# Kernel tuning notes

Hardware: AMD Instinct MI355X
Metric: run time of the kernel (lower is better)

Reference implementation:

```python
import jax, jax.numpy as jnp
import numpy as np

B, S, E, H, D = 8, 1024, 1024, 16, 64
LN_EPS = 1e-5


def setup_inputs() -> dict:
    key = jax.random.key(0)
    ks = jax.random.split(key, 8)
    scale = 1.0 / np.sqrt(E)
    return {
        "query": jax.random.normal(ks[0], (B, S, E), jnp.float32),
        "key": jax.random.normal(ks[1], (B, S, E), jnp.float32),
        "value": jax.random.normal(ks[2], (B, S, E), jnp.float32),
        "self_attn_mask": jax.random.randint(ks[3], (B, S, S), 0, 2) == 1,
        "Wq": jax.random.normal(ks[4], (E, H * D), jnp.float32) * scale,
        "Wk": jax.random.normal(ks[5], (E, H * D), jnp.float32) * scale,
        "Wv": jax.random.normal(ks[6], (E, H * D), jnp.float32) * scale,
        "Wo": jax.random.normal(ks[7], (H * D, E), jnp.float32) * scale,
        "ln_gamma": jnp.ones((E,), jnp.float32),
        "ln_beta": jnp.zeros((E,), jnp.float32),
    }


def reference(query, key, value, self_attn_mask, Wq, Wk, Wv, Wo, ln_gamma, ln_beta):
    identity = query
    # project and split heads: [B, S, E] -> [B, H, S, D]
    q = (query @ Wq).reshape(B, S, H, D).transpose(0, 2, 1, 3)
    k = (key @ Wk).reshape(B, S, H, D).transpose(0, 2, 1, 3)
    v = (value @ Wv).reshape(B, S, H, D).transpose(0, 2, 1, 3)
    # scaled dot-product scores in fp32, additive mask fill -1e9
    score = jnp.einsum("bhsd,bhtd->bhst", q, k).astype(jnp.float32) / np.sqrt(D)
    score = jnp.where(self_attn_mask[:, None, :, :], jnp.float32(-1e9), score)
    attn = jax.nn.softmax(score, axis=-1)
    degree = jnp.einsum("bhst,bhtd->bhsd", attn, v)  # [B, H, S, D]
    degree = degree.transpose(0, 2, 1, 3).reshape(B, S, H * D)
    out = degree @ Wo + identity
    # LayerNorm over last dim
    mu = jnp.mean(out, axis=-1, keepdims=True)
    var = jnp.var(out, axis=-1, keepdims=True)
    out = (out - mu) * jax.lax.rsqrt(var + LN_EPS) * ln_gamma + ln_beta
    return out
```

## Files before the change

### kernel.cpp

```cpp
#include <hip/hip_runtime.h>
#include <hip/hip_bf16.h>
#include <cstdint>
#include <cstddef>

typedef __attribute__((ext_vector_type(8))) short bf16x8;
typedef __attribute__((ext_vector_type(8))) unsigned short ushort8;
typedef __attribute__((ext_vector_type(4))) unsigned short ushort4v;
typedef __attribute__((ext_vector_type(4))) float f32x4;

#define B_ 8
#define S_ 1024
#define E_ 1024
#define H_ 16
#define D_ 64
#define NW_ (S_ / 64)

__device__ __forceinline__ unsigned short f2bf(float f) {
    union { float fp; unsigned int u; } v; v.fp = f;
    unsigned int u = v.u;
    return (unsigned short)((u + 0x7fffu + ((u >> 16) & 1u)) >> 16);
}

__device__ __forceinline__ float fexp2(float x) {
    return __builtin_amdgcn_exp2f(x);
}

__device__ __forceinline__ unsigned cvt_pk_bf16(float lo, float hi) {
    unsigned r;
    asm("v_cvt_pk_bf16_f32 %0, %1, %2" : "=v"(r) : "v"(lo), "v"(hi));
    return r;
}

__device__ __forceinline__ void gload16(const void* g, void* l) {
    __builtin_amdgcn_global_load_lds((__attribute__((address_space(1))) void*)g,
                                     (__attribute__((address_space(3))) void*)l,
                                     16, 0, 0);
}

__global__ __launch_bounds__(256) void f32_to_bf16(const float* __restrict__ in,
                                                   unsigned short* __restrict__ out,
                                                   int n8) {
    int i = blockIdx.x * 256 + threadIdx.x;
    const int stride = gridDim.x * 256;
    for (; i < n8; i += stride) {
        float4 f0 = ((const float4*)in)[i * 2];
        float4 f1 = ((const float4*)in)[i * 2 + 1];
        union { unsigned u[4]; ushort8 v; } o;
        o.u[0] = cvt_pk_bf16(f0.x, f0.y);
        o.u[1] = cvt_pk_bf16(f0.z, f0.w);
        o.u[2] = cvt_pk_bf16(f1.x, f1.y);
        o.u[3] = cvt_pk_bf16(f1.z, f1.w);
        ((ushort8*)out)[i] = o.v;
    }
}

__global__ __launch_bounds__(256) void wtrans4(const float* __restrict__ W0,
                                               const float* __restrict__ W1,
                                               const float* __restrict__ W2,
                                               const float* __restrict__ W3,
                                               unsigned short* __restrict__ T0,
                                               unsigned short* __restrict__ T1,
                                               unsigned short* __restrict__ T2,
                                               unsigned short* __restrict__ T3) {
    const float* W = (blockIdx.z == 0) ? W0 : (blockIdx.z == 1) ? W1 : (blockIdx.z == 2) ? W2 : W3;
    unsigned short* Wt = (blockIdx.z == 0) ? T0 : (blockIdx.z == 1) ? T1 : (blockIdx.z == 2) ? T2 : T3;
    __shared__ float tile[32][33];
    const int k0 = blockIdx.y * 32, n0 = blockIdx.x * 32;
    const int tx = threadIdx.x & 31, ty = threadIdx.x >> 5;
#pragma unroll
    for (int i = ty; i < 32; i += 8)
        tile[i][tx] = W[(size_t)(k0 + i) * E_ + n0 + tx];
    __syncthreads();
#pragma unroll
    for (int i = ty; i < 32; i += 8)
        Wt[(size_t)(n0 + i) * E_ + k0 + tx] = f2bf(tile[tx][i]);
}

__global__ void detect_kernel(const unsigned int* __restrict__ m, int* __restrict__ flag) {
    unsigned int bad = 0;
    for (int i = threadIdx.x; i < 4096; i += 64) bad |= (m[i] > 1u) ? 1u : 0u;
    unsigned long long anybad = __ballot(bad != 0u);
    if (threadIdx.x == 0) *flag = (anybad == 0ull) ? 1 : 0;
}

__global__ __launch_bounds__(256) void pack_mask(const void* __restrict__ maskp,
                                                 const int* __restrict__ flagp,
                                                 unsigned long long* __restrict__ mbits) {
    const int mask32 = *flagp;
    const int lane = threadIdx.x & 63;
    const int gw = blockIdx.x * 4 + (threadIdx.x >> 6);
    const int nwaves = gridDim.x * 4;
    const int totw = B_ * S_ * NW_;
    for (int w = gw; w < totw; w += nwaves) {
        bool m;
        if (mask32) m = ((const int*)maskp)[(size_t)w * 64 + lane] != 0;
        else        m = ((const unsigned char*)maskp)[(size_t)w * 64 + lane] != 0;
        unsigned long long bits = __ballot(m);
        if (lane == 0) mbits[w] = bits;
    }
}

template <int EPI>
__global__ __launch_bounds__(256) void gemm_bt(const unsigned short* __restrict__ A,
                                               const unsigned short* __restrict__ Bt,
                                               void* __restrict__ Cp,
                                               const float* __restrict__ resid,
                                               float cscale) {
    __shared__ unsigned short As[128 * 32];
    __shared__ unsigned short Bs[128 * 32];
    const int t = threadIdx.x;
    const int lane = t & 63, w = t >> 6;
    const int wr = w >> 1, wc = w & 1;
    const int l15 = lane & 15, l4 = lane >> 4;
    const int m0 = blockIdx.x * 128, n0 = blockIdx.y * 128;

    const int srow = w * 32 + (lane >> 2);
    const int scol = (lane & 3) * 8;
    const unsigned short* Ag0 = A + (size_t)(m0 + srow) * E_ + scol;
    const unsigned short* Ag1 = A + (size_t)(m0 + srow + 16) * E_ + scol;
    const unsigned short* Bg0 = Bt + (size_t)(n0 + srow) * E_ + scol;
    const unsigned short* Bg1 = Bt + (size_t)(n0 + srow + 16) * E_ + scol;
    unsigned short* Al = &As[w * 1024];
    unsigned short* Bl = &Bs[w * 1024];

    f32x4 acc[4][4];
#pragma unroll
    for (int i = 0; i < 4; ++i)
#pragma unroll
        for (int j = 0; j < 4; ++j) acc[i][j] = (f32x4){0.f, 0.f, 0.f, 0.f};

    for (int kt = 0; kt < E_; kt += 32) {
        gload16(Ag0 + kt, Al);
        gload16(Ag1 + kt, Al + 512);
        gload16(Bg0 + kt, Bl);
        gload16(Bg1 + kt, Bl + 512);
        __syncthreads();
        bf16x8 af[4], bfv[4];
#pragma unroll
        for (int mi = 0; mi < 4; ++mi)
            af[mi] = *(const bf16x8*)&As[(wr * 64 + mi * 16 + l15) * 32 + l4 * 8];
#pragma unroll
        for (int ni = 0; ni < 4; ++ni)
            bfv[ni] = *(const bf16x8*)&Bs[(wc * 64 + ni * 16 + l15) * 32 + l4 * 8];
#pragma unroll
        for (int mi = 0; mi < 4; ++mi)
#pragma unroll
            for (int ni = 0; ni < 4; ++ni)
                acc[mi][ni] =
                    __builtin_amdgcn_mfma_f32_16x16x32_bf16(af[mi], bfv[ni], acc[mi][ni], 0, 0, 0);
        __syncthreads();
    }
#pragma unroll
    for (int mi = 0; mi < 4; ++mi) {
#pragma unroll
        for (int ni = 0; ni < 4; ++ni) {
#pragma unroll
            for (int r = 0; r < 4; ++r) {
                const int m = m0 + wr * 64 + mi * 16 + l4 * 4 + r;
                const int n = n0 + wc * 64 + ni * 16 + l15;
                const float v = acc[mi][ni][r];
                if (EPI == 0) {
                    const int b = m >> 10, s = m & 1023, h = n >> 6, d = n & 63;
                    ((unsigned short*)Cp)[(((size_t)b * H_ + h) * S_ + s) * D_ + d] = f2bf(v * cscale);
                } else if (EPI == 2) {
                    const int b = m >> 10, s = m & 1023, h = n >> 6, d = n & 63;
                    ((unsigned short*)Cp)[(((size_t)b * H_ + h) * D_ + d) * S_ + s] = f2bf(v);
                } else {
                    const size_t idx = (size_t)m * E_ + n;
                    ((float*)Cp)[idx] = v + resid[idx];
                }
            }
        }
    }
}

__global__ __launch_bounds__(256) void attn_kernel(const unsigned short* __restrict__ Qh,
                                                   const unsigned short* __restrict__ Kh,
                                                   const unsigned short* __restrict__ Vt,
                                                   const unsigned long long* __restrict__ mbits,
                                                   unsigned short* __restrict__ degree) {
    __shared__ unsigned short Ks[64 * 64];
    __shared__ unsigned short Vs[64 * 64];
    __shared__ unsigned short Ps[4 * 16 * 64];
    const int t = threadIdx.x;
    const int lane = t & 63, w = t >> 6;
    const int l15 = lane & 15, l4 = lane >> 4;
    const int i = blockIdx.x;
    const int L = (i & 7) * 256 + (i >> 3);
    const int bh = L >> 4, b = bh >> 4, h = bh & 15;
    const int q0 = (L & 15) * 64;
    const int myq = q0 + w * 16 + l15;

    const unsigned long long* mrow = mbits + ((size_t)b * S_ + myq) * NW_;

    bf16x8 qf[2];
    {
        const unsigned short* qptr = Qh + ((size_t)bh * S_ + myq) * D_ + l4 * 8;
        qf[0] = *(const bf16x8*)qptr;
        qf[1] = *(const bf16x8*)(qptr + 32);
    }
    f32x4 O[4];
#pragma unroll
    for (int idx = 0; idx < 4; ++idx) O[idx] = (f32x4){0.f, 0.f, 0.f, 0.f};
    float mrun = -3e38f, lrun = 0.f;

    const int srow = t >> 2, sch = (t & 3) * 2;
    const int ssw = (srow & 7) << 4;
    char* KsB = (char*)Ks;
    char* VsB = (char*)Vs;
    char* PsB = (char*)Ps + w * 2048;
    const int psw = (l15 & 7) << 4;

    for (int jt = 0; jt < S_; jt += 64) {
        {
            const unsigned short* kg = Kh + ((size_t)bh * S_ + jt + srow) * D_ + sch * 8;
            *(ushort8*)(KsB + srow * 128 + ((sch * 16) ^ ssw)) = *(const ushort8*)kg;
            *(ushort8*)(KsB + srow * 128 + ((sch * 16 + 16) ^ ssw)) = *(const ushort8*)(kg + 8);
            const unsigned short* vg = Vt + ((size_t)bh * D_ + srow) * S_ + jt + sch * 8;
            *(ushort8*)(VsB + srow * 128 + ((sch * 16) ^ ssw)) = *(const ushort8*)vg;
            *(ushort8*)(VsB + srow * 128 + ((sch * 16 + 16) ^ ssw)) = *(const ushort8*)(vg + 8);
        }
        const unsigned long long mw = mrow[jt >> 6];
        __syncthreads();

        f32x4 sacc[4];
#pragma unroll
        for (int idx = 0; idx < 4; ++idx) sacc[idx] = (f32x4){0.f, 0.f, 0.f, 0.f};
#pragma unroll
        for (int ni = 0; ni < 4; ++ni) {
            const int row = l15 + ni * 16;
            const int sw = (row & 7) << 4;
            bf16x8 b0 = *(const bf16x8*)(KsB + row * 128 + ((l4 * 16) ^ sw));
            bf16x8 b1 = *(const bf16x8*)(KsB + row * 128 + ((64 + l4 * 16) ^ sw));
            sacc[ni] = __builtin_amdgcn_mfma_f32_16x16x32_bf16(b0, qf[0], sacc[ni], 0, 0, 0);
            sacc[ni] = __builtin_amdgcn_mfma_f32_16x16x32_bf16(b1, qf[1], sacc[ni], 0, 0, 0);
        }

        float m0 = -3e38f;
#pragma unroll
        for (int ni = 0; ni < 4; ++ni) {
#pragma unroll
            for (int r = 0; r < 4; ++r) {
                const int k = ni * 16 + l4 * 4 + r;
                const float s = ((mw >> k) & 1ull) ? -1e9f : sacc[ni][r];
                sacc[ni][r] = s;
                m0 = fmaxf(m0, s);
            }
        }
        m0 = fmaxf(m0, __shfl_xor(m0, 16, 64));
        m0 = fmaxf(m0, __shfl_xor(m0, 32, 64));
        if (!__all(m0 <= mrun + 8.f)) {
            const float mnew = fmaxf(mrun, m0);
            const float corr = fexp2(mrun - mnew);
            lrun *= corr;
#pragma unroll
            for (int df = 0; df < 4; ++df)
#pragma unroll
                for (int r = 0; r < 4; ++r) O[df][r] *= corr;
            mrun = mnew;
        }
        float ps = 0.f;
#pragma unroll
        for (int ni = 0; ni < 4; ++ni) {
            float p0 = fexp2(sacc[ni][0] - mrun);
            float p1 = fexp2(sacc[ni][1] - mrun);
            float p2 = fexp2(sacc[ni][2] - mrun);
            float p3 = fexp2(sacc[ni][3] - mrun);
            ps += (p0 + p1) + (p2 + p3);
            uint2 pw;
            pw.x = cvt_pk_bf16(p0, p1);
            pw.y = cvt_pk_bf16(p2, p3);
            *(uint2*)(PsB + l15 * 128 + ((ni * 32 + l4 * 8) ^ psw)) = pw;
        }
        ps += __shfl_xor(ps, 16, 64);
        ps += __shfl_xor(ps, 32, 64);
        lrun += ps;

        asm volatile("s_waitcnt lgkmcnt(0)" ::: "memory");
        bf16x8 pa0 = *(const bf16x8*)(PsB + l15 * 128 + ((l4 * 16) ^ psw));
        bf16x8 pa1 = *(const bf16x8*)(PsB + l15 * 128 + ((64 + l4 * 16) ^ psw));
#pragma unroll
        for (int df = 0; df < 4; ++df) {
            const int row = l15 + df * 16;
            const int sw = (row & 7) << 4;
            bf16x8 v0 = *(const bf16x8*)(VsB + row * 128 + ((l4 * 16) ^ sw));
            bf16x8 v1 = *(const bf16x8*)(VsB + row * 128 + ((64 + l4 * 16) ^ sw));
            O[df] = __builtin_amdgcn_mfma_f32_16x16x32_bf16(v0, pa0, O[df], 0, 0, 0);
            O[df] = __builtin_amdgcn_mfma_f32_16x16x32_bf16(v1, pa1, O[df], 0, 0, 0);
        }
        __syncthreads();
    }

    const float inv = 1.f / lrun;
#pragma unroll
    for (int df = 0; df < 4; ++df) {
        ushort4v ow;
#pragma unroll
        for (int r = 0; r < 4; ++r) ow[r] = f2bf(O[df][r] * inv);
        const size_t dst = ((size_t)b * S_ + myq) * (size_t)(H_ * D_) +
                           h * 64 + df * 16 + l4 * 4;
        *(ushort4v*)(degree + dst) = ow;
    }
}

__global__ __launch_bounds__(256) void lnorm(float* __restrict__ io,
                                             const float* __restrict__ gamma,
                                             const float* __restrict__ beta) {
    const int row = blockIdx.x;
    const int t = threadIdx.x;
    float4 v = ((const float4*)(io + (size_t)row * E_))[t];
    float s = v.x + v.y + v.z + v.w;
    float q = v.x * v.x + v.y * v.y + v.z * v.z + v.w * v.w;
#pragma unroll
    for (int off = 32; off; off >>= 1) {
        s += __shfl_down(s, off, 64);
        q += __shfl_down(q, off, 64);
    }
    __shared__ float red[8];
    const int wid = t >> 6;
    if ((t & 63) == 0) { red[wid] = s; red[4 + wid] = q; }
    __syncthreads();
    const float ts = red[0] + red[1] + red[2] + red[3];
    const float tq = red[4] + red[5] + red[6] + red[7];
    const float mean = ts * (1.0f / E_);
    const float var = tq * (1.0f / E_) - mean * mean;
    const float rstd = rsqrtf(var + 1e-5f);
    const float4 g = ((const float4*)gamma)[t];
    const float4 bb = ((const float4*)beta)[t];
    v.x = (v.x - mean) * rstd * g.x + bb.x;
    v.y = (v.y - mean) * rstd * g.y + bb.y;
    v.z = (v.z - mean) * rstd * g.z + bb.z;
    v.w = (v.w - mean) * rstd * g.w + bb.w;
    ((float4*)(io + (size_t)row * E_))[t] = v;
}

extern "C" void kernel_launch(void* const* d_in, const int* in_sizes, int n_in,
                              void* d_out, int out_size, void* d_ws, size_t ws_size,
                              hipStream_t stream) {
    const float* query = (const float*)d_in[0];
    const float* key_ = (const float*)d_in[1];
    const float* value = (const float*)d_in[2];
    const void* maskp = d_in[3];
    const float* Wq = (const float*)d_in[4];
    const float* Wk = (const float*)d_in[5];
    const float* Wv = (const float*)d_in[6];
    const float* Wo = (const float*)d_in[7];
    const float* gamma = (const float*)d_in[8];
    const float* beta = (const float*)d_in[9];
    float* out = (float*)d_out;
    char* ws = (char*)d_ws;
    const size_t MB = 1024ull * 1024ull;

    unsigned short* WqT = (unsigned short*)(ws + 0 * MB);
    unsigned short* WkT = (unsigned short*)(ws + 2 * MB);
    unsigned short* WvT = (unsigned short*)(ws + 4 * MB);
    unsigned short* WoT = (unsigned short*)(ws + 6 * MB);
    unsigned short* Qh = (unsigned short*)(ws + 8 * MB);
    unsigned short* Kh = (unsigned short*)(ws + 24 * MB);
    unsigned short* Vt = (unsigned short*)(ws + 40 * MB);
    unsigned short* deg = (unsigned short*)(ws + 56 * MB);
    unsigned short* Abf = deg;
    int* flag = (int*)(ws + 72 * MB);
    unsigned long long* mbits = (unsigned long long*)(ws + 72 * MB + 4096);

    const int n8 = B_ * S_ * E_ / 8;
    const float qscale = 0.125f * 1.4426950408889634f;

    wtrans4<<<dim3(32, 32, 4), 256, 0, stream>>>(Wq, Wk, Wv, Wo, WqT, WkT, WvT, WoT);
    detect_kernel<<<1, 64, 0, stream>>>((const unsigned int*)maskp, flag);
    pack_mask<<<2048, 256, 0, stream>>>(maskp, flag, mbits);

    f32_to_bf16<<<2048, 256, 0, stream>>>(query, Abf, n8);
    gemm_bt<0><<<dim3(64, 8), 256, 0, stream>>>(Abf, WqT, Qh, nullptr, qscale);
    f32_to_bf16<<<2048, 256, 0, stream>>>(key_, Abf, n8);
    gemm_bt<0><<<dim3(64, 8), 256, 0, stream>>>(Abf, WkT, Kh, nullptr, 1.0f);
    f32_to_bf16<<<2048, 256, 0, stream>>>(value, Abf, n8);
    gemm_bt<2><<<dim3(64, 8), 256, 0, stream>>>(Abf, WvT, Vt, nullptr, 1.0f);

    attn_kernel<<<2048, 256, 0, stream>>>(Qh, Kh, Vt, mbits, deg);

    gemm_bt<3><<<dim3(64, 8), 256, 0, stream>>>(deg, WoT, out, query, 1.0f);
    lnorm<<<8192, 256, 0, stream>>>(out, gamma, beta);
}
```

Measured before the change: 253.0 us.

## Deepen GEMM K-tile with swizzled LDS and prefetch K/V tiles in attention

The GEMM now stages 64-wide K slices per iteration with an XOR-swizzled LDS layout, halving the number of barrier pairs and aiming to reduce bank conflicts. The attention kernel loads the next K/V tile into registers while the current tile is computed, so global latency overlaps with MFMA and softmax work, and it uses a raw s_barrier with explicit waitcnt. The max and sum reductions are also split into shorter dependency chains. This costs double the GEMM shared memory and more live registers, which may reduce occupancy.

Result: faster. 246.9 us (-2.4%).

```diff
diff --git a/kernel.cpp b/kernel.cpp
--- a/kernel.cpp
+++ b/kernel.cpp
@@ -106,22 +106,25 @@
                                                void* __restrict__ Cp,
                                                const float* __restrict__ resid,
                                                float cscale) {
-    __shared__ unsigned short As[128 * 32];
-    __shared__ unsigned short Bs[128 * 32];
+    __shared__ unsigned short As[128 * 64];
+    __shared__ unsigned short Bs[128 * 64];
     const int t = threadIdx.x;
     const int lane = t & 63, w = t >> 6;
     const int wr = w >> 1, wc = w & 1;
     const int l15 = lane & 15, l4 = lane >> 4;
     const int m0 = blockIdx.x * 128, n0 = blockIdx.y * 128;
 
-    const int srow = w * 32 + (lane >> 2);
-    const int scol = (lane & 3) * 8;
-    const unsigned short* Ag0 = A + (size_t)(m0 + srow) * E_ + scol;
-    const unsigned short* Ag1 = A + (size_t)(m0 + srow + 16) * E_ + scol;
-    const unsigned short* Bg0 = Bt + (size_t)(n0 + srow) * E_ + scol;
-    const unsigned short* Bg1 = Bt + (size_t)(n0 + srow + 16) * E_ + scol;
-    unsigned short* Al = &As[w * 1024];
-    unsigned short* Bl = &Bs[w * 1024];
+    const int lr = lane >> 3, lc = lane & 7;
+    const int csrc = (lc ^ lr) * 8;
+    const unsigned short* Ag[4];
+    const unsigned short* Bg[4];
+#pragma unroll
+    for (int g = 0; g < 4; ++g) {
+        Ag[g] = A + (size_t)(m0 + w * 32 + g * 8 + lr) * E_ + csrc;
+        Bg[g] = Bt + (size_t)(n0 + w * 32 + g * 8 + lr) * E_ + csrc;
+    }
+    unsigned short* Al = &As[w * 32 * 64];
+    unsigned short* Bl = &Bs[w * 32 * 64];
 
     f32x4 acc[4][4];
 #pragma unroll
@@ -129,25 +132,35 @@
 #pragma unroll
         for (int j = 0; j < 4; ++j) acc[i][j] = (f32x4){0.f, 0.f, 0.f, 0.f};
 
-    for (int kt = 0; kt < E_; kt += 32) {
-        gload16(Ag0 + kt, Al);
-        gload16(Ag1 + kt, Al + 512);
-        gload16(Bg0 + kt, Bl);
-        gload16(Bg1 + kt, Bl + 512);
+    const int r7 = (l15 & 7) << 4;
+    const char* AsB = (const char*)As;
+    const char* BsB = (const char*)Bs;
+
+    for (int kt = 0; kt < E_; kt += 64) {
+#pragma unroll
+        for (int g = 0; g < 4; ++g) {
+            gload16(Ag[g] + kt, Al + g * 512);
+            gload16(Bg[g] + kt, Bl + g * 512);
+        }
         __syncthreads();
-        bf16x8 af[4], bfv[4];
-#pragma unroll
-        for (int mi = 0; mi < 4; ++mi)
-            af[mi] = *(const bf16x8*)&As[(wr * 64 + mi * 16 + l15) * 32 + l4 * 8];
-#pragma unroll
-        for (int ni = 0; ni < 4; ++ni)
-            bfv[ni] = *(const bf16x8*)&Bs[(wc * 64 + ni * 16 + l15) * 32 + l4 * 8];
-#pragma unroll
-        for (int mi = 0; mi < 4; ++mi)
+#pragma unroll
+        for (int kk = 0; kk < 2; ++kk) {
+            bf16x8 af[4], bfv[4];
+#pragma unroll
+            for (int mi = 0; mi < 4; ++mi)
+                af[mi] = *(const bf16x8*)(AsB + (size_t)(wr * 64 + mi * 16 + l15) * 128 +
+                                          ((((kk * 4 + l4) << 4)) ^ r7));
 #pragma unroll
             for (int ni = 0; ni < 4; ++ni)
-                acc[mi][ni] =
-                    __builtin_amdgcn_mfma_f32_16x16x32_bf16(af[mi], bfv[ni], acc[mi][ni], 0, 0, 0);
+                bfv[ni] = *(const bf16x8*)(BsB + (size_t)(wc * 64 + ni * 16 + l15) * 128 +
+                                           ((((kk * 4 + l4) << 4)) ^ r7));
+#pragma unroll
+            for (int mi = 0; mi < 4; ++mi)
+#pragma unroll
+                for (int ni = 0; ni < 4; ++ni)
+                    acc[mi][ni] = __builtin_amdgcn_mfma_f32_16x16x32_bf16(af[mi], bfv[ni],
+                                                                          acc[mi][ni], 0, 0, 0);
+        }
         __syncthreads();
     }
 #pragma unroll
@@ -211,17 +224,28 @@
     char* PsB = (char*)Ps + w * 2048;
     const int psw = (l15 & 7) << 4;
 
+    const unsigned short* kgb = Kh + ((size_t)bh * S_ + srow) * D_ + sch * 8;
+    const unsigned short* vgb = Vt + ((size_t)bh * D_ + srow) * S_ + sch * 8;
+
+    ushort8 kp0 = *(const ushort8*)kgb;
+    ushort8 kp1 = *(const ushort8*)(kgb + 8);
+    ushort8 vp0 = *(const ushort8*)vgb;
+    ushort8 vp1 = *(const ushort8*)(vgb + 8);
+
     for (int jt = 0; jt < S_; jt += 64) {
-        {
-            const unsigned short* kg = Kh + ((size_t)bh * S_ + jt + srow) * D_ + sch * 8;
-            *(ushort8*)(KsB + srow * 128 + ((sch * 16) ^ ssw)) = *(const ushort8*)kg;
-            *(ushort8*)(KsB + srow * 128 + ((sch * 16 + 16) ^ ssw)) = *(const ushort8*)(kg + 8);
-            const unsigned short* vg = Vt + ((size_t)bh * D_ + srow) * S_ + jt + sch * 8;
-            *(ushort8*)(VsB + srow * 128 + ((sch * 16) ^ ssw)) = *(const ushort8*)vg;
-            *(ushort8*)(VsB + srow * 128 + ((sch * 16 + 16) ^ ssw)) = *(const ushort8*)(vg + 8);
-        }
         const unsigned long long mw = mrow[jt >> 6];
-        __syncthreads();
+        *(ushort8*)(KsB + srow * 128 + ((sch * 16) ^ ssw)) = kp0;
+        *(ushort8*)(KsB + srow * 128 + ((sch * 16 + 16) ^ ssw)) = kp1;
+        *(ushort8*)(VsB + srow * 128 + ((sch * 16) ^ ssw)) = vp0;
+        *(ushort8*)(VsB + srow * 128 + ((sch * 16 + 16) ^ ssw)) = vp1;
+        if (jt + 64 < S_) {
+            kp0 = *(const ushort8*)(kgb + (size_t)(jt + 64) * D_);
+            kp1 = *(const ushort8*)(kgb + (size_t)(jt + 64) * D_ + 8);
+            vp0 = *(const ushort8*)(vgb + jt + 64);
+            vp1 = *(const ushort8*)(vgb + jt + 64 + 8);
+        }
+        asm volatile("s_waitcnt lgkmcnt(0)" ::: "memory");
+        __builtin_amdgcn_s_barrier();
 
         f32x4 sacc[4];
 #pragma unroll
@@ -236,17 +260,18 @@
             sacc[ni] = __builtin_amdgcn_mfma_f32_16x16x32_bf16(b1, qf[1], sacc[ni], 0, 0, 0);
         }
 
-        float m0 = -3e38f;
+        float gmax[4];
 #pragma unroll
         for (int ni = 0; ni < 4; ++ni) {
-#pragma unroll
-            for (int r = 0; r < 4; ++r) {
-                const int k = ni * 16 + l4 * 4 + r;
-                const float s = ((mw >> k) & 1ull) ? -1e9f : sacc[ni][r];
-                sacc[ni][r] = s;
-                m0 = fmaxf(m0, s);
-            }
-        }
+            const int kbase = ni * 16 + l4 * 4;
+            float s0 = ((mw >> (kbase + 0)) & 1ull) ? -1e9f : sacc[ni][0];
+            float s1 = ((mw >> (kbase + 1)) & 1ull) ? -1e9f : sacc[ni][1];
+            float s2 = ((mw >> (kbase + 2)) & 1ull) ? -1e9f : sacc[ni][2];
+            float s3 = ((mw >> (kbase + 3)) & 1ull) ? -1e9f : sacc[ni][3];
+            sacc[ni][0] = s0; sacc[ni][1] = s1; sacc[ni][2] = s2; sacc[ni][3] = s3;
+            gmax[ni] = fmaxf(fmaxf(s0, s1), fmaxf(s2, s3));
+        }
+        float m0 = fmaxf(fmaxf(gmax[0], gmax[1]), fmaxf(gmax[2], gmax[3]));
         m0 = fmaxf(m0, __shfl_xor(m0, 16, 64));
         m0 = fmaxf(m0, __shfl_xor(m0, 32, 64));
         if (!__all(m0 <= mrun + 8.f)) {
@@ -259,19 +284,20 @@
                 for (int r = 0; r < 4; ++r) O[df][r] *= corr;
             mrun = mnew;
         }
-        float ps = 0.f;
+        float psn[4];
 #pragma unroll
         for (int ni = 0; ni < 4; ++ni) {
             float p0 = fexp2(sacc[ni][0] - mrun);
             float p1 = fexp2(sacc[ni][1] - mrun);
             float p2 = fexp2(sacc[ni][2] - mrun);
             float p3 = fexp2(sacc[ni][3] - mrun);
-            ps += (p0 + p1) + (p2 + p3);
+            psn[ni] = (p0 + p1) + (p2 + p3);
             uint2 pw;
             pw.x = cvt_pk_bf16(p0, p1);
             pw.y = cvt_pk_bf16(p2, p3);
             *(uint2*)(PsB + l15 * 128 + ((ni * 32 + l4 * 8) ^ psw)) = pw;
         }
+        float ps = (psn[0] + psn[1]) + (psn[2] + psn[3]);
         ps += __shfl_xor(ps, 16, 64);
         ps += __shfl_xor(ps, 32, 64);
         lrun += ps;
@@ -288,7 +314,7 @@
             O[df] = __builtin_amdgcn_mfma_f32_16x16x32_bf16(v0, pa0, O[df], 0, 0, 0);
             O[df] = __builtin_amdgcn_mfma_f32_16x16x32_bf16(v1, pa1, O[df], 0, 0, 0);
         }
-        __syncthreads();
+        __builtin_amdgcn_s_barrier();
     }
 
     const float inv = 1.f / lrun;
```
